# Optimization experiments

Hardware: AMD Instinct MI355X
Metric: run time of the kernel (lower is better)

Reference implementation:

```python
import jax, jax.numpy as jnp
import numpy as np

NL = 4      # num_hidden_layers
NH = 12     # self-attn heads
CH = 4      # cross-attn heads (hardcoded in module)
S = 4       # speakers per dialog
EPS = 1e-5

def layernorm(x, g, b):
    m = x.mean(-1, keepdims=True)
    v = jnp.mean((x - m) ** 2, axis=-1, keepdims=True)
    return (x - m) * jax.lax.rsqrt(v + EPS) * g + b

def self_mha(x, in_w, in_b, out_w, out_b):
    # x: [B,T,L,H] self-attention over L (the per-turn token axis)
    B, T, L, H = x.shape
    dh = H // NH
    qkv = x @ in_w + in_b                       # [B,T,L,3H]
    q, k, v = jnp.split(qkv, 3, axis=-1)
    q = q.reshape(B, T, L, NH, dh); k = k.reshape(B, T, L, NH, dh); v = v.reshape(B, T, L, NH, dh)
    s = jnp.einsum('btqhd,btkhd->bthqk', q, k) / np.sqrt(dh).astype(x.dtype)
    a = jax.nn.softmax(s, axis=-1)
    o = jnp.einsum('bthqk,btkhd->btqhd', a, v).reshape(B, T, L, H)
    return o @ out_w + out_b

def forward(input_ids, attention_mask, speaker_ids, tok_emb, pos_emb, turn_emb,
            mha_in_w, mha_in_b, mha_out_w, mha_out_b,
            ffn_w1, ffn_b1, ffn_w2, ffn_b2,
            ln1_g, ln1_b, ln2_g, ln2_b,
            gate_w, gate_b, sn_g, sn_b,
            ca_in_w, ca_in_b, ca_out_w, ca_out_b):
    B, T, L = input_ids.shape
    H = tok_emb.shape[1]
    X = tok_emb[input_ids] + pos_emb[jnp.arange(L)][None, None] + turn_emb[jnp.arange(T)][None, :, None]
    mask = attention_mask[..., None].astype(X.dtype)            # [B,T,L,1]
    onehot = (speaker_ids[..., None] == jnp.arange(S)).astype(X.dtype)  # [B,T,S]
    counts = onehot.sum(1)                                      # [B,S]
    M = jnp.zeros((B, S, H), X.dtype)                           # speaker memory
    for l in range(NL):
        m_t = jnp.einsum('bts,bsh->bth', onehot, M)             # gather memory per turn
        h = (X + m_t[:, :, None, :]) * mask                     # mask applied by zeroing inputs (as in source)
        h = self_mha(h, mha_in_w[l], mha_in_b[l], mha_out_w[l], mha_out_b[l])
        h = layernorm(h + X, ln1_g[l], ln1_b[l])
        ffn = jax.nn.gelu(h @ ffn_w1[l] + ffn_b1[l], approximate=False) @ ffn_w2[l] + ffn_b2[l]
        h = layernorm(h + ffn, ln2_g[l], ln2_b[l])
        X = h
        tc = h.mean(2)                                          # token_context [B,T,H]
        # cross-attention: each turn's context queries its dialog's speaker memory
        wq, wk, wv = jnp.split(ca_in_w[l], 3, axis=-1)
        bq, bk, bv = jnp.split(ca_in_b[l], 3)
        dh = H // CH
        q = (tc @ wq + bq).reshape(B, T, CH, dh)
        k = (M @ wk + bk).reshape(B, S, CH, dh)
        v = (M @ wv + bv).reshape(B, S, CH, dh)
        s = jnp.einsum('bthd,bshd->bhts', q, k) / np.sqrt(dh).astype(X.dtype)
        a = jax.nn.softmax(s, axis=-1)
        cc = jnp.einsum('bhts,bshd->bthd', a, v).reshape(B, T, H) @ ca_out_w[l] + ca_out_b[l]
        fused = jnp.concatenate([tc, m_t, cc], axis=-1)         # [B,T,3H]
        upd = layernorm(fused @ gate_w[l] + gate_b[l] + m_t, sn_g[l], sn_b[l])
        # scatter: per-speaker mean over that speaker's turns; untouched speakers keep old memory
        sums = jnp.einsum('bts,bth->bsh', onehot, upd)
        mean = sums / jnp.maximum(counts, 1.0)[..., None]
        M = jnp.where((counts > 0)[..., None], mean, M)
    return X, M

def setup_inputs() -> dict:
    key = jax.random.key(0)
    ks = iter(jax.random.split(key, 32))
    B, T, L, H, F, V, P = 8, 64, 64, 768, 3072, 30522, 512
    n = lambda shape: jax.random.normal(next(ks), shape, jnp.float32) * 0.02
    return {
        'input_ids': jax.random.randint(next(ks), (B, T, L), 0, V, jnp.int32),
        'attention_mask': jax.random.randint(next(ks), (B, T, L), 0, 2, jnp.int32),
        'speaker_ids': jax.random.randint(next(ks), (B, T), 0, S, jnp.int32),
        'tok_emb': n((V, H)), 'pos_emb': n((P, H)), 'turn_emb': n((P, H)),
        'mha_in_w': n((NL, H, 3 * H)), 'mha_in_b': jnp.zeros((NL, 3 * H)),
        'mha_out_w': n((NL, H, H)), 'mha_out_b': jnp.zeros((NL, H)),
        'ffn_w1': n((NL, H, F)), 'ffn_b1': jnp.zeros((NL, F)),
        'ffn_w2': n((NL, F, H)), 'ffn_b2': jnp.zeros((NL, H)),
        'ln1_g': jnp.ones((NL, H)), 'ln1_b': jnp.zeros((NL, H)),
        'ln2_g': jnp.ones((NL, H)), 'ln2_b': jnp.zeros((NL, H)),
        'gate_w': n((NL, 3 * H, H)), 'gate_b': jnp.zeros((NL, H)),
        'sn_g': jnp.ones((NL, H)), 'sn_b': jnp.zeros((NL, H)),
        'ca_in_w': n((NL, H, 3 * H)), 'ca_in_b': jnp.zeros((NL, 3 * H)),
        'ca_out_w': n((NL, H, H)), 'ca_out_b': jnp.zeros((NL, H)),
    }

def reference(input_ids, attention_mask, speaker_ids, tok_emb, pos_emb, turn_emb,
              mha_in_w, mha_in_b, mha_out_w, mha_out_b,
              ffn_w1, ffn_b1, ffn_w2, ffn_b2,
              ln1_g, ln1_b, ln2_g, ln2_b,
              gate_w, gate_b, sn_g, sn_b,
              ca_in_w, ca_in_b, ca_out_w, ca_out_b):
    return forward(input_ids, attention_mask, speaker_ids, tok_emb, pos_emb, turn_emb,
                   mha_in_w, mha_in_b, mha_out_w, mha_out_b,
                   ffn_w1, ffn_b1, ffn_w2, ffn_b2,
                   ln1_g, ln1_b, ln2_g, ln2_b,
                   gate_w, gate_b, sn_g, sn_b,
                   ca_in_w, ca_in_b, ca_out_w, ca_out_b)
```

## Files before the change

kernel.cpp:

```cpp
#include <hip/hip_runtime.h>

using u16 = unsigned short;
using u32 = unsigned int;

#define DI __device__ __forceinline__

typedef __bf16 bf16x8 __attribute__((ext_vector_type(8)));
typedef float  f32x4  __attribute__((ext_vector_type(4)));

DI float b2f(u16 u){ u32 x = ((u32)u) << 16; float f; __builtin_memcpy(&f, &x, 4); return f; }
DI u16 f2b(float f){ __bf16 h = (__bf16)f; u16 r; __builtin_memcpy(&r, &h, 2); return r; }
DI float gelu_fast(float v){
    float u = v * (0.7978845608f + 0.0356774081f * v * v);
    float e = __expf(2.0f * u);
    float t = 1.0f - 2.0f / (e + 1.0f);
    return 0.5f * v * (1.0f + t);
}

#define GLOAD16(g, l) __builtin_amdgcn_global_load_lds( \
    (const __attribute__((address_space(1))) void*)(g), \
    (__attribute__((address_space(3))) void*)(l), 16, 0, 0)

DI bf16x8 ldsr128(const u16* p) {
    bf16x8 r;
    asm volatile("ds_read_b128 %0, %1"
                 : "=v"(r)
                 : "v"((const __attribute__((address_space(3))) u16*)p));
    return r;
}

template<int EPI>
__global__ __launch_bounds__(512, 2)
void gemm256(const u16* __restrict__ A, const u16* __restrict__ Bt,
             const float* __restrict__ bias, void* __restrict__ Cout,
             int M, int N, int K)
{
    __shared__ u16 lA[3][256 * 32];
    __shared__ u16 lB[3][256 * 32];
    const int tid  = threadIdx.x;
    const int lane = tid & 63;
    const int w    = tid >> 6;
    const int wm   = w >> 2, wn = w & 3;

    const int nx = gridDim.x;
    const int nb = nx * gridDim.y;
    int bid = blockIdx.y * nx + blockIdx.x;
    if ((nb & 7) == 0) bid = ((bid & 7) * (nb >> 3)) + (bid >> 3);
    const int m0 = (bid / nx) * 256;
    const int n0 = (bid % nx) * 256;

    f32x4 acc[8][4] = {};

    const int srow = tid >> 2;
    const int scol = (((tid & 3) ^ ((tid >> 3) & 3)) * 8);
    int ar0 = m0 + srow;       if (ar0 > M - 1) ar0 = M - 1;
    int ar1 = m0 + 128 + srow; if (ar1 > M - 1) ar1 = M - 1;
    const u16* gA0 = A  + (size_t)ar0 * K + scol;
    const u16* gA1 = A  + (size_t)ar1 * K + scol;
    const u16* gB0 = Bt + (size_t)(n0 + srow) * K + scol;
    const u16* gB1 = Bt + (size_t)(n0 + 128 + srow) * K + scol;

    const int la = lane & 15, lg = lane >> 4;
    const int cp = (lg ^ ((la >> 1) & 3)) * 8;

    const int nt = K >> 5;

    #define STAGE256(buf, koff) do { \
        GLOAD16(gA0 + (koff), &lA[buf][tid * 8]); \
        GLOAD16(gA1 + (koff), &lA[buf][4096 + tid * 8]); \
        GLOAD16(gB0 + (koff), &lB[buf][tid * 8]); \
        GLOAD16(gB1 + (koff), &lB[buf][4096 + tid * 8]); \
    } while (0)

    STAGE256(0, 0);
    STAGE256(1, 32);

    int cur = 0, pre = 2;
    for (int t = 0; t < nt; ++t) {
        if (t + 1 < nt) asm volatile("s_waitcnt vmcnt(4)" ::: "memory");
        else            asm volatile("s_waitcnt vmcnt(0)" ::: "memory");
        __builtin_amdgcn_s_barrier();
        asm volatile("" ::: "memory");

        if (t + 2 < nt) STAGE256(pre, (t + 2) << 5);

        bf16x8 af[8], bfr[4];
        #pragma unroll
        for (int i = 0; i < 8; i++)
            af[i] = ldsr128(&lA[cur][(wm * 128 + i * 16 + la) * 32 + cp]);
        #pragma unroll
        for (int j = 0; j < 4; j++)
            bfr[j] = ldsr128(&lB[cur][(wn * 64 + j * 16 + la) * 32 + cp]);
        asm volatile("s_waitcnt lgkmcnt(0)" ::: "memory");
        __builtin_amdgcn_sched_barrier(0);

        __builtin_amdgcn_s_setprio(1);
        #pragma unroll
        for (int i = 0; i < 8; i++)
            #pragma unroll
            for (int j = 0; j < 4; j++)
                acc[i][j] = __builtin_amdgcn_mfma_f32_16x16x32_bf16(af[i], bfr[j], acc[i][j], 0, 0, 0);
        __builtin_amdgcn_s_setprio(0);

        cur = (cur == 2) ? 0 : cur + 1;
        pre = (pre == 2) ? 0 : pre + 1;
    }
    #undef STAGE256

    #pragma unroll
    for (int i = 0; i < 8; i++) {
        const int rowb = m0 + wm * 128 + i * 16 + lg * 4;
        #pragma unroll
        for (int j = 0; j < 4; j++) {
            const int col = n0 + wn * 64 + j * 16 + la;
            const float bv = bias[col];
            #pragma unroll
            for (int r = 0; r < 4; r++) {
                const int rr = rowb + r;
                if (rr < M) {
                    float v = acc[i][j][r] + bv;
                    if constexpr (EPI == 1) v = gelu_fast(v);
                    if constexpr (EPI == 2) ((float*)Cout)[(size_t)rr * N + col] = v;
                    else                    ((u16*)Cout)[(size_t)rr * N + col] = f2b(v);
                }
            }
        }
    }
}

template<int EPI>
__global__ __launch_bounds__(256)
void gemm_bt(const u16* __restrict__ A, const u16* __restrict__ Bt,
             const float* __restrict__ bias, void* __restrict__ Cout,
             int M, int N, int K)
{
    __shared__ u16 lA[3][128 * 32];
    __shared__ u16 lB[3][128 * 32];
    const int tid  = threadIdx.x;
    const int lane = tid & 63;
    const int w    = tid >> 6;
    const int wm   = w >> 1, wn = w & 1;

    const int nx = gridDim.x;
    const int nb = nx * gridDim.y;
    int bid = blockIdx.y * nx + blockIdx.x;
    if ((nb & 7) == 0) bid = ((bid & 7) * (nb >> 3)) + (bid >> 3);
    const int m0 = (bid / nx) * 128;
    const int n0 = (bid % nx) * 128;

    f32x4 acc[4][4] = {};

    const int srow = tid >> 2;
    const int scol = (((tid & 3) ^ ((tid >> 3) & 3)) * 8);
    int ar0 = m0 + srow;      if (ar0 > M - 1) ar0 = M - 1;
    int ar1 = m0 + 64 + srow; if (ar1 > M - 1) ar1 = M - 1;
    const u16* gA0 = A  + (size_t)ar0 * K + scol;
    const u16* gA1 = A  + (size_t)ar1 * K + scol;
    const u16* gB0 = Bt + (size_t)(n0 + srow) * K + scol;
    const u16* gB1 = Bt + (size_t)(n0 + 64 + srow) * K + scol;

    const int la = lane & 15, lg = lane >> 4;
    const int cp = (lg ^ ((la >> 1) & 3)) * 8;

    const int nt = K >> 5;

    GLOAD16(gA0,      &lA[0][tid * 8]);
    GLOAD16(gA1,      &lA[0][tid * 8 + 2048]);
    GLOAD16(gB0,      &lB[0][tid * 8]);
    GLOAD16(gB1,      &lB[0][tid * 8 + 2048]);
    GLOAD16(gA0 + 32, &lA[1][tid * 8]);
    GLOAD16(gA1 + 32, &lA[1][tid * 8 + 2048]);
    GLOAD16(gB0 + 32, &lB[1][tid * 8]);
    GLOAD16(gB1 + 32, &lB[1][tid * 8 + 2048]);

    int cur = 0, pre = 2;
    for (int t = 0; t < nt; ++t) {
        if (t + 1 < nt) asm volatile("s_waitcnt vmcnt(4)" ::: "memory");
        else            asm volatile("s_waitcnt vmcnt(0)" ::: "memory");
        __builtin_amdgcn_s_barrier();
        asm volatile("" ::: "memory");

        if (t + 2 < nt) {
            const int k0 = (t + 2) << 5;
            GLOAD16(gA0 + k0, &lA[pre][tid * 8]);
            GLOAD16(gA1 + k0, &lA[pre][tid * 8 + 2048]);
            GLOAD16(gB0 + k0, &lB[pre][tid * 8]);
            GLOAD16(gB1 + k0, &lB[pre][tid * 8 + 2048]);
        }

        bf16x8 af[4], bfr[4];
        #pragma unroll
        for (int i = 0; i < 4; i++)
            af[i] = ldsr128(&lA[cur][(wm * 64 + i * 16 + la) * 32 + cp]);
        #pragma unroll
        for (int j = 0; j < 4; j++)
            bfr[j] = ldsr128(&lB[cur][(wn * 64 + j * 16 + la) * 32 + cp]);
        asm volatile("s_waitcnt lgkmcnt(0)" ::: "memory");
        __builtin_amdgcn_sched_barrier(0);

        #pragma unroll
        for (int i = 0; i < 4; i++)
            #pragma unroll
            for (int j = 0; j < 4; j++)
                acc[i][j] = __builtin_amdgcn_mfma_f32_16x16x32_bf16(af[i], bfr[j], acc[i][j], 0, 0, 0);

        cur = (cur == 2) ? 0 : cur + 1;
        pre = (pre == 2) ? 0 : pre + 1;
    }

    #pragma unroll
    for (int i = 0; i < 4; i++) {
        const int rowb = m0 + wm * 64 + i * 16 + lg * 4;
        #pragma unroll
        for (int j = 0; j < 4; j++) {
            const int col = n0 + wn * 64 + j * 16 + la;
            const float bv = bias[col];
            #pragma unroll
            for (int r = 0; r < 4; r++) {
                const int rr = rowb + r;
                if (rr < M) {
                    float v = acc[i][j][r] + bv;
                    if constexpr (EPI == 1) v = gelu_fast(v);
                    if constexpr (EPI == 2) ((float*)Cout)[(size_t)rr * N + col] = v;
                    else                    ((u16*)Cout)[(size_t)rr * N + col] = f2b(v);
                }
            }
        }
    }
}

__global__ __launch_bounds__(256)
void transp_conv(const float* __restrict__ in, u16* __restrict__ out, int K, int N)
{
    __shared__ float tile[32][33];
    const int l = blockIdx.z;
    const float* inp = in + (size_t)l * K * N;
    u16* op = out + (size_t)l * K * N;
    const int kb = blockIdx.y * 32, nb = blockIdx.x * 32;
    const int tx = threadIdx.x, ty = threadIdx.y;
    #pragma unroll
    for (int i = 0; i < 32; i += 8)
        tile[ty + i][tx] = inp[(size_t)(kb + ty + i) * N + nb + tx];
    __syncthreads();
    #pragma unroll
    for (int i = 0; i < 32; i += 8)
        op[(size_t)(nb + ty + i) * K + kb + tx] = f2b(tile[tx][ty + i]);
}

__global__ __launch_bounds__(192)
void embed_k(const int* __restrict__ ids, const float* __restrict__ te,
             const float* __restrict__ pe, const float* __restrict__ ue,
             u16* __restrict__ X)
{
    const int tok = blockIdx.x;
    const int l = tok & 63;
    const int t = (tok >> 6) & 63;
    const int id = ids[tok];
    const int c = threadIdx.x * 4;
    float4 a = *(const float4*)&te[(size_t)id * 768 + c];
    float4 p = *(const float4*)&pe[(size_t)l * 768 + c];
    float4 u = *(const float4*)&ue[(size_t)t * 768 + c];
    ushort4 o;
    o.x = f2b(a.x + p.x + u.x); o.y = f2b(a.y + p.y + u.y);
    o.z = f2b(a.z + p.z + u.z); o.w = f2b(a.w + p.w + u.w);
    *(ushort4*)&X[(size_t)tok * 768 + c] = o;
}

__global__ __launch_bounds__(256)
void gather_mt(const float* __restrict__ M, const int* __restrict__ sid,
               float* __restrict__ mt)
{
    const int bt = blockIdx.x, b = bt >> 6, tid = threadIdx.x;
    const float* src = M + ((size_t)b * 4 + sid[bt]) * 768;
    float* dst = mt + (size_t)bt * 768;
    dst[tid] = src[tid]; dst[tid + 256] = src[tid + 256]; dst[tid + 512] = src[tid + 512];
}

__global__ __launch_bounds__(192)
void prep_ain(const u16* __restrict__ X, const float* __restrict__ mt,
              const int* __restrict__ mask, u16* __restrict__ Ain)
{
    const int tok = blockIdx.x, bt = tok >> 6;
    const float mk = (float)mask[tok];
    const int c = threadIdx.x * 4;
    ushort4 xv = *(const ushort4*)&X[(size_t)tok * 768 + c];
    float4 mv = *(const float4*)&mt[(size_t)bt * 768 + c];
    ushort4 o;
    o.x = f2b((b2f(xv.x) + mv.x) * mk); o.y = f2b((b2f(xv.y) + mv.y) * mk);
    o.z = f2b((b2f(xv.z) + mv.z) * mk); o.w = f2b((b2f(xv.w) + mv.w) * mk);
    *(ushort4*)&Ain[(size_t)tok * 768 + c] = o;
}

DI int swz(int row, int col) { return row * 64 + (((col >> 3) ^ (row & 7)) << 3) + (col & 7); }

__global__ __launch_bounds__(256)
void attn_self(const u16* __restrict__ QKV, u16* __restrict__ O)
{
    __shared__ u16 lQ[64 * 64], lK[64 * 64], lVt[64 * 64], lP[64 * 64];
    __shared__ float lS[64 * 68];
    const int bt = blockIdx.x / 12, h = blockIdx.x % 12;
    const int tid = threadIdx.x, lane = tid & 63, w = tid >> 6;
    const size_t base = (size_t)bt * 64 * 2304;

    #pragma unroll
    for (int it = 0; it < 2; ++it) {
        const int slot = it * 256 + tid;
        const int l = slot >> 3, dc = (slot & 7) * 8;
        const u16* qp = QKV + base + (size_t)l * 2304 + h * 64 + dc;
        *(uint4*)&lQ[swz(l, dc)] = *(const uint4*)qp;
        *(uint4*)&lK[swz(l, dc)] = *(const uint4*)(qp + 768);
        uint4 vv = *(const uint4*)(qp + 1536);
        u16 tmp[8]; *(uint4*)tmp = vv;
        #pragma unroll
        for (int j = 0; j < 8; j++) lVt[swz(dc + j, l)] = tmp[j];
    }
    __syncthreads();

    const int la = lane & 15, lg = lane >> 4;
    {
        f32x4 sa[4] = {};
        #pragma unroll
        for (int kh = 0; kh < 64; kh += 32) {
            bf16x8 aq = *(const bf16x8*)&lQ[swz(w * 16 + la, kh + lg * 8)];
            #pragma unroll
            for (int fn = 0; fn < 4; ++fn) {
                bf16x8 bk = *(const bf16x8*)&lK[swz(fn * 16 + la, kh + lg * 8)];
                sa[fn] = __builtin_amdgcn_mfma_f32_16x16x32_bf16(aq, bk, sa[fn], 0, 0, 0);
            }
        }
        #pragma unroll
        for (int fn = 0; fn < 4; ++fn)
            #pragma unroll
            for (int r = 0; r < 4; ++r)
                lS[(w * 16 + lg * 4 + r) * 68 + fn * 16 + la] = sa[fn][r] * 0.125f;
    }
    __syncthreads();

    {
        const int row = tid >> 2, q4 = tid & 3;
        float e[16]; float mx = -1e30f;
        #pragma unroll
        for (int j = 0; j < 16; j++) { e[j] = lS[row * 68 + q4 * 16 + j]; mx = fmaxf(mx, e[j]); }
        mx = fmaxf(mx, __shfl_xor(mx, 1)); mx = fmaxf(mx, __shfl_xor(mx, 2));
        float sm = 0.f;
        #pragma unroll
        for (int j = 0; j < 16; j++) { e[j] = __expf(e[j] - mx); sm += e[j]; }
        sm += __shfl_xor(sm, 1); sm += __shfl_xor(sm, 2);
        const float inv = 1.0f / sm;
        #pragma unroll
        for (int j = 0; j < 16; j++) lP[swz(row, q4 * 16 + j)] = f2b(e[j] * inv);
    }
    __syncthreads();

    {
        f32x4 oa[4] = {};
        #pragma unroll
        for (int kh = 0; kh < 64; kh += 32) {
            bf16x8 ap = *(const bf16x8*)&lP[swz(w * 16 + la, kh + lg * 8)];
            #pragma unroll
            for (int fn = 0; fn < 4; ++fn) {
                bf16x8 bv = *(const bf16x8*)&lVt[swz(fn * 16 + la, kh + lg * 8)];
                oa[fn] = __builtin_amdgcn_mfma_f32_16x16x32_bf16(ap, bv, oa[fn], 0, 0, 0);
            }
        }
        const size_t ob = (size_t)bt * 64 * 768 + h * 64;
        #pragma unroll
        for (int fn = 0; fn < 4; ++fn)
            #pragma unroll
            for (int r = 0; r < 4; ++r)
                O[ob + (size_t)(w * 16 + lg * 4 + r) * 768 + fn * 16 + la] = f2b(oa[fn][r]);
    }
}

DI float wave_red(float v) {
    #pragma unroll
    for (int o = 32; o > 0; o >>= 1) v += __shfl_xor(v, o);
    return v;
}

__global__ __launch_bounds__(256)
void ln_res(const u16* __restrict__ a, const u16* __restrict__ b,
            const float* __restrict__ g, const float* __restrict__ be,
            u16* __restrict__ out)
{
    __shared__ float red[8];
    const int tid = threadIdx.x;
    const size_t off = (size_t)blockIdx.x * 768;
    float x0 = b2f(a[off + tid])       + b2f(b[off + tid]);
    float x1 = b2f(a[off + tid + 256]) + b2f(b[off + tid + 256]);
    float x2 = b2f(a[off + tid + 512]) + b2f(b[off + tid + 512]);
    float s = wave_red(x0 + x1 + x2);
    float ss = wave_red(x0 * x0 + x1 * x1 + x2 * x2);
    if ((tid & 63) == 0) { red[tid >> 6] = s; red[4 + (tid >> 6)] = ss; }
    __syncthreads();
    s = red[0] + red[1] + red[2] + red[3];
    ss = red[4] + red[5] + red[6] + red[7];
    const float mean = s * (1.f / 768.f);
    const float var = fmaxf(ss * (1.f / 768.f) - mean * mean, 0.f);
    const float inv = rsqrtf(var + 1e-5f);
    out[off + tid]       = f2b((x0 - mean) * inv * g[tid]       + be[tid]);
    out[off + tid + 256] = f2b((x1 - mean) * inv * g[tid + 256] + be[tid + 256]);
    out[off + tid + 512] = f2b((x2 - mean) * inv * g[tid + 512] + be[tid + 512]);
}

__global__ __launch_bounds__(256)
void ln_upd(const float* __restrict__ a, const float* __restrict__ b,
            const float* __restrict__ g, const float* __restrict__ be,
            float* __restrict__ out)
{
    __shared__ float red[8];
    const int tid = threadIdx.x;
    const size_t off = (size_t)blockIdx.x * 768;
    float x0 = a[off + tid]       + b[off + tid];
    float x1 = a[off + tid + 256] + b[off + tid + 256];
    float x2 = a[off + tid + 512] + b[off + tid + 512];
    float s = wave_red(x0 + x1 + x2);
    float ss = wave_red(x0 * x0 + x1 * x1 + x2 * x2);
    if ((tid & 63) == 0) { red[tid >> 6] = s; red[4 + (tid >> 6)] = ss; }
    __syncthreads();
    s = red[0] + red[1] + red[2] + red[3];
    ss = red[4] + red[5] + red[6] + red[7];
    const float mean = s * (1.f / 768.f);
    const float var = fmaxf(ss * (1.f / 768.f) - mean * mean, 0.f);
    const float inv = rsqrtf(var + 1e-5f);
    out[off + tid]       = (x0 - mean) * inv * g[tid]       + be[tid];
    out[off + tid + 256] = (x1 - mean) * inv * g[tid + 256] + be[tid + 256];
    out[off + tid + 512] = (x2 - mean) * inv * g[tid + 512] + be[tid + 512];
}

__global__ __launch_bounds__(256)
void tc_mean(const u16* __restrict__ X, u16* __restrict__ tcb)
{
    const int bt = blockIdx.x, tid = threadIdx.x;
    float s0 = 0, s1 = 0, s2 = 0;
    for (int l = 0; l < 64; ++l) {
        const u16* r = X + ((size_t)bt * 64 + l) * 768;
        s0 += b2f(r[tid]); s1 += b2f(r[tid + 256]); s2 += b2f(r[tid + 512]);
    }
    tcb[(size_t)bt * 768 + tid]       = f2b(s0 * (1.f / 64.f));
    tcb[(size_t)bt * 768 + tid + 256] = f2b(s1 * (1.f / 64.f));
    tcb[(size_t)bt * 768 + tid + 512] = f2b(s2 * (1.f / 64.f));
}

__global__ __launch_bounds__(256)
void conv_bf16(const float* __restrict__ in, u16* __restrict__ out, int n)
{
    const int i = blockIdx.x * 256 + threadIdx.x;
    if (i < n) out[i] = f2b(in[i]);
}

__global__ __launch_bounds__(256)
void zero_f32(float* __restrict__ buf, int n)
{
    const int i = blockIdx.x * 256 + threadIdx.x;
    if (i < n) buf[i] = 0.f;
}

__global__ __launch_bounds__(256)
void cross_attn(const u16* __restrict__ qc, const u16* __restrict__ kvc,
                u16* __restrict__ cca)
{
    __shared__ float q[768], kk[4][768], vv[4][768], sraw[16], aw[16];
    const int bt = blockIdx.x, b = bt >> 6, tid = threadIdx.x;
    #pragma unroll
    for (int i = 0; i < 3; i++) q[tid + i * 256] = b2f(qc[(size_t)bt * 768 + tid + i * 256]);
    #pragma unroll
    for (int i = 0; i < 12; i++) {
        const int idx = i * 256 + tid;
        const int s = idx / 768, d = idx % 768;
        kk[s][d] = b2f(kvc[(size_t)(b * 4 + s) * 1536 + d]);
        vv[s][d] = b2f(kvc[(size_t)(b * 4 + s) * 1536 + 768 + d]);
    }
    __syncthreads();
    if (tid < 16) {
        const int hh = tid >> 2, s = tid & 3;
        float acc = 0.f;
        for (int d = 0; d < 192; ++d) acc += q[hh * 192 + d] * kk[s][hh * 192 + d];
        sraw[tid] = acc * 0.07216878364870323f;
    }
    __syncthreads();
    if (tid < 4) {
        float m = -1e30f;
        for (int s = 0; s < 4; s++) m = fmaxf(m, sraw[tid * 4 + s]);
        float ee[4], sm = 0.f;
        for (int s = 0; s < 4; s++) { ee[s] = __expf(sraw[tid * 4 + s] - m); sm += ee[s]; }
        for (int s = 0; s < 4; s++) aw[tid * 4 + s] = ee[s] / sm;
    }
    __syncthreads();
    #pragma unroll
    for (int i = 0; i < 3; i++) {
        const int j = tid + i * 256;
        const int hh = j / 192;
        float v = aw[hh * 4 + 0] * vv[0][j] + aw[hh * 4 + 1] * vv[1][j]
                + aw[hh * 4 + 2] * vv[2][j] + aw[hh * 4 + 3] * vv[3][j];
        cca[(size_t)bt * 768 + j] = f2b(v);
    }
}

__global__ __launch_bounds__(256)
void concat_fused(const u16* __restrict__ tcb, const float* __restrict__ mt,
                  const u16* __restrict__ ccp, u16* __restrict__ Fu)
{
    const int bt = blockIdx.x, tid = threadIdx.x;
    u16* o = Fu + (size_t)bt * 2304;
    #pragma unroll
    for (int i = 0; i < 3; i++) {
        const int j = tid + i * 256;
        o[j]        = tcb[(size_t)bt * 768 + j];
        o[768 + j]  = f2b(mt[(size_t)bt * 768 + j]);
        o[1536 + j] = ccp[(size_t)bt * 768 + j];
    }
}

__global__ __launch_bounds__(256)
void scatter_mem(const float* __restrict__ upd, const int* __restrict__ sid,
                 const float* __restrict__ counts, float* __restrict__ M)
{
    const int bs = blockIdx.x, b = bs >> 2, s = bs & 3, tid = threadIdx.x;
    const float c = counts[bs];
    #pragma unroll
    for (int i = 0; i < 3; i++) {
        const int j = tid + i * 256;
        float acc = 0.f;
        for (int t = 0; t < 64; ++t)
            if (sid[b * 64 + t] == s) acc += upd[((size_t)b * 64 + t) * 768 + j];
        if (c > 0.f) M[(size_t)bs * 768 + j] = acc / fmaxf(c, 1.f);
    }
}

__global__ void calc_counts(const int* __restrict__ sid, float* __restrict__ counts)
{
    const int tid = threadIdx.x;
    if (tid < 32) {
        const int b = tid >> 2, s = tid & 3;
        float c = 0.f;
        for (int t = 0; t < 64; ++t) c += (sid[b * 64 + t] == s) ? 1.f : 0.f;
        counts[tid] = c;
    }
}

__global__ __launch_bounds__(256)
void final_out(const u16* __restrict__ Xb, const float* __restrict__ M,
               float* __restrict__ out)
{
    const size_t i = (size_t)blockIdx.x * 256 + threadIdx.x;
    const size_t NX = 25165824ull;
    if (i < NX) out[i] = b2f(Xb[i]);
    else if (i < NX + 24576ull) out[i] = M[i - NX];
}

extern "C" void kernel_launch(void* const* d_in, const int* in_sizes, int n_in,
                              void* d_out, int out_size, void* d_ws, size_t ws_size,
                              hipStream_t stream)
{
    const int*   input_ids = (const int*)d_in[0];
    const int*   attn_mask = (const int*)d_in[1];
    const int*   sid       = (const int*)d_in[2];
    const float* tok_emb   = (const float*)d_in[3];
    const float* pos_emb   = (const float*)d_in[4];
    const float* turn_emb  = (const float*)d_in[5];
    const float* mha_in_w  = (const float*)d_in[6];
    const float* mha_in_b  = (const float*)d_in[7];
    const float* mha_out_w = (const float*)d_in[8];
    const float* mha_out_b = (const float*)d_in[9];
    const float* ffn_w1    = (const float*)d_in[10];
    const float* ffn_b1    = (const float*)d_in[11];
    const float* ffn_w2    = (const float*)d_in[12];
    const float* ffn_b2    = (const float*)d_in[13];
    const float* ln1_g     = (const float*)d_in[14];
    const float* ln1_b     = (const float*)d_in[15];
    const float* ln2_g     = (const float*)d_in[16];
    const float* ln2_b     = (const float*)d_in[17];
    const float* gate_w    = (const float*)d_in[18];
    const float* gate_b    = (const float*)d_in[19];
    const float* sn_g      = (const float*)d_in[20];
    const float* sn_b      = (const float*)d_in[21];
    const float* ca_in_w   = (const float*)d_in[22];
    const float* ca_in_b   = (const float*)d_in[23];
    const float* ca_out_w  = (const float*)d_in[24];
    const float* ca_out_b  = (const float*)d_in[25];
    (void)in_sizes; (void)n_in; (void)out_size;

    const size_t MB = 1ull << 20;
    int NCA, NCF; bool allW;
    if      (ws_size >= 460 * MB) { NCA = 2; NCF = 1; allW = true;  }
    else if (ws_size >= 255 * MB) { NCA = 2; NCF = 2; allW = false; }
    else                          { NCA = 4; NCF = 4; allW = false; }
    const int MRA = 32768 / NCA;
    const int MRF = 32768 / NCF;
    const size_t wl = allW ? 4 : 1;

    char* p = (char*)d_ws;
    auto alloc = [&](size_t n) { void* r = p; p += (n + 255) & ~(size_t)255; return r; };
    u16*   Xb    = (u16*)alloc(50331648);
    u16*   Hb    = (u16*)alloc(50331648);
    u16*   WqkvT = (u16*)alloc(wl * 3538944);
    u16*   WoT   = (u16*)alloc(wl * 1179648);
    u16*   W1T   = (u16*)alloc(wl * 4718592);
    u16*   W2T   = (u16*)alloc(wl * 4718592);
    u16*   WgT   = (u16*)alloc(wl * 3538944);
    u16*   WcaT  = (u16*)alloc(wl * 3538944);
    u16*   WcoT  = (u16*)alloc(wl * 1179648);
    float* mt    = (float*)alloc(1572864);
    u16*   tcb   = (u16*)alloc(786432);
    u16*   Mb    = (u16*)alloc(49152);
    u16*   qc    = (u16*)alloc(786432);
    u16*   kvc   = (u16*)alloc(98304);
    u16*   cca   = (u16*)alloc(786432);
    u16*   ccp   = (u16*)alloc(786432);
    u16*   Fu    = (u16*)alloc(2359296);
    float* gout  = (float*)alloc(1572864);
    float* upd   = (float*)alloc(1572864);
    float* cnts  = (float*)alloc(256);
    float* M     = (float*)alloc(98304);

    u16 *A, *QKVb, *Gb;
    if (NCF == 1) {
        A    = (u16*)alloc(50331648);
        Gb   = (u16*)alloc(201326592);
        QKVb = (u16*)d_out;
    } else if (NCF == 2) {
        A    = (u16*)alloc(50331648);
        QKVb = (u16*)alloc((size_t)MRA * 2304 * 2);
        Gb   = (u16*)d_out;
    } else {
        Gb   = (u16*)alloc((size_t)MRF * 3072 * 2);
        A    = (u16*)d_out;
        QKVb = (u16*)d_out + 25165824;
    }
    u16* Obuf = Gb;

    zero_f32<<<96, 256, 0, stream>>>(M, 24576);
    calc_counts<<<1, 64, 0, stream>>>(sid, cnts);
    embed_k<<<32768, 192, 0, stream>>>(input_ids, tok_emb, pos_emb, turn_emb, Xb);

    if (allW) {
        transp_conv<<<dim3(72, 24, 4), dim3(32, 8), 0, stream>>>(mha_in_w,  WqkvT, 768, 2304);
        transp_conv<<<dim3(24, 24, 4), dim3(32, 8), 0, stream>>>(mha_out_w, WoT,   768, 768);
        transp_conv<<<dim3(96, 24, 4), dim3(32, 8), 0, stream>>>(ffn_w1,    W1T,   768, 3072);
        transp_conv<<<dim3(24, 96, 4), dim3(32, 8), 0, stream>>>(ffn_w2,    W2T,  3072, 768);
        transp_conv<<<dim3(24, 72, 4), dim3(32, 8), 0, stream>>>(gate_w,    WgT,  2304, 768);
        transp_conv<<<dim3(72, 24, 4), dim3(32, 8), 0, stream>>>(ca_in_w,   WcaT,  768, 2304);
        transp_conv<<<dim3(24, 24, 4), dim3(32, 8), 0, stream>>>(ca_out_w,  WcoT,  768, 768);
    }

    for (int l = 0; l < 4; ++l) {
        if (!allW) {
            transp_conv<<<dim3(72, 24), dim3(32, 8), 0, stream>>>(mha_in_w  + (size_t)l * 768 * 2304, WqkvT, 768, 2304);
            transp_conv<<<dim3(24, 24), dim3(32, 8), 0, stream>>>(mha_out_w + (size_t)l * 768 * 768,  WoT,   768, 768);
            transp_conv<<<dim3(96, 24), dim3(32, 8), 0, stream>>>(ffn_w1    + (size_t)l * 768 * 3072, W1T,   768, 3072);
            transp_conv<<<dim3(24, 96), dim3(32, 8), 0, stream>>>(ffn_w2    + (size_t)l * 3072 * 768, W2T,  3072, 768);
            transp_conv<<<dim3(24, 72), dim3(32, 8), 0, stream>>>(gate_w    + (size_t)l * 2304 * 768, WgT,  2304, 768);
            transp_conv<<<dim3(72, 24), dim3(32, 8), 0, stream>>>(ca_in_w   + (size_t)l * 768 * 2304, WcaT,  768, 2304);
            transp_conv<<<dim3(24, 24), dim3(32, 8), 0, stream>>>(ca_out_w  + (size_t)l * 768 * 768,  WcoT,  768, 768);
        }
        const u16* Wqkv_l = WqkvT + (size_t)(allW ? l : 0) * 2304 * 768;
        const u16* Wo_l   = WoT   + (size_t)(allW ? l : 0) * 768 * 768;
        const u16* W1_l   = W1T   + (size_t)(allW ? l : 0) * 768 * 3072;
        const u16* W2_l   = W2T   + (size_t)(allW ? l : 0) * 3072 * 768;
        const u16* Wg_l   = WgT   + (size_t)(allW ? l : 0) * 2304 * 768;
        const u16* Wca_l  = WcaT  + (size_t)(allW ? l : 0) * 768 * 2304;
        const u16* Wco_l  = WcoT  + (size_t)(allW ? l : 0) * 768 * 768;

        gather_mt<<<512, 256, 0, stream>>>(M, sid, mt);
        prep_ain<<<32768, 192, 0, stream>>>(Xb, mt, attn_mask, A);

        for (int c = 0; c < NCA; ++c) {
            u16* Ac = A + (size_t)c * MRA * 768;
            gemm256<0><<<dim3(9, MRA / 256), 512, 0, stream>>>(Ac, Wqkv_l, mha_in_b + l * 2304, QKVb, MRA, 2304, 768);
            attn_self<<<(MRA / 64) * 12, 256, 0, stream>>>(QKVb, Obuf);
            gemm256<0><<<dim3(3, MRA / 256), 512, 0, stream>>>(Obuf, Wo_l, mha_out_b + l * 768, Ac, MRA, 768, 768);
        }
        ln_res<<<32768, 256, 0, stream>>>(A, Xb, ln1_g + l * 768, ln1_b + l * 768, Hb);

        for (int c = 0; c < NCF; ++c) {
            u16* Hc = Hb + (size_t)c * MRF * 768;
            u16* Ac = A  + (size_t)c * MRF * 768;
            gemm256<1><<<dim3(12, MRF / 256), 512, 0, stream>>>(Hc, W1_l, ffn_b1 + l * 3072, Gb, MRF, 3072, 768);
            gemm256<0><<<dim3(3, MRF / 256), 512, 0, stream>>>(Gb, W2_l, ffn_b2 + l * 768, Ac, MRF, 768, 3072);
        }
        ln_res<<<32768, 256, 0, stream>>>(A, Hb, ln2_g + l * 768, ln2_b + l * 768, Xb);

        tc_mean<<<512, 256, 0, stream>>>(Xb, tcb);
        conv_bf16<<<96, 256, 0, stream>>>(M, Mb, 24576);
        gemm_bt<0><<<dim3(6, 4), 256, 0, stream>>>(tcb, Wca_l, ca_in_b + l * 2304, qc, 512, 768, 768);
        gemm_bt<0><<<dim3(12, 1), 256, 0, stream>>>(Mb, Wca_l + 768 * 768, ca_in_b + l * 2304 + 768, kvc, 32, 1536, 768);
        cross_attn<<<512, 256, 0, stream>>>(qc, kvc, cca);
        gemm_bt<0><<<dim3(6, 4), 256, 0, stream>>>(cca, Wco_l, ca_out_b + l * 768, ccp, 512, 768, 768);
        concat_fused<<<512, 256, 0, stream>>>(tcb, mt, ccp, Fu);
        gemm_bt<2><<<dim3(6, 4), 256, 0, stream>>>(Fu, Wg_l, gate_b + l * 768, gout, 512, 768, 2304);
        ln_upd<<<512, 256, 0, stream>>>(gout, mt, sn_g + l * 768, sn_b + l * 768, upd);
        scatter_mem<<<32, 256, 0, stream>>>(upd, sid, cnts, M);
    }

    final_out<<<98400, 256, 0, stream>>>(Xb, M, (float*)d_out);
}
```

Measured before the change: 4.256 ms.

## Switch gemm256 to BK=64 double-buffered LDS pipeline with 8-way swizzle

The GEMM mainloop moves from a triple-buffered 32-wide K tile to a double-buffered 64-wide K tile. Each iteration now issues two MFMA sub-steps per barrier, and the LDS layout uses a 3-bit XOR swizzle on 64-element rows. The aim is to halve the number of barriers and loop iterations and to raise global load granularity. LDS use rises to 128KB per block, which forces launch_bounds occupancy down to 1 block per CU. A full vmcnt(0) wait each iteration removes the two-deep prefetch slack the old version had.

Result: no change. 4.208 ms (-1.1%).

```diff
diff --git a/kernel.cpp b/kernel.cpp
--- a/kernel.cpp
+++ b/kernel.cpp
@@ -30,13 +30,13 @@
 }
 
 template<int EPI>
-__global__ __launch_bounds__(512, 2)
+__global__ __launch_bounds__(512, 1)
 void gemm256(const u16* __restrict__ A, const u16* __restrict__ Bt,
              const float* __restrict__ bias, void* __restrict__ Cout,
              int M, int N, int K)
 {
-    __shared__ u16 lA[3][256 * 32];
-    __shared__ u16 lB[3][256 * 32];
+    __shared__ u16 lA[2][256 * 64];
+    __shared__ u16 lB[2][256 * 64];
     const int tid  = threadIdx.x;
     const int lane = tid & 63;
     const int w    = tid >> 6;
@@ -51,61 +51,64 @@
 
     f32x4 acc[8][4] = {};
 
-    const int srow = tid >> 2;
-    const int scol = (((tid & 3) ^ ((tid >> 3) & 3)) * 8);
-    int ar0 = m0 + srow;       if (ar0 > M - 1) ar0 = M - 1;
-    int ar1 = m0 + 128 + srow; if (ar1 > M - 1) ar1 = M - 1;
-    const u16* gA0 = A  + (size_t)ar0 * K + scol;
-    const u16* gA1 = A  + (size_t)ar1 * K + scol;
-    const u16* gB0 = Bt + (size_t)(n0 + srow) * K + scol;
-    const u16* gB1 = Bt + (size_t)(n0 + 128 + srow) * K + scol;
+    const int srowb = w * 32 + (lane >> 3);
+    const int csrc  = ((lane & 7) ^ ((lane >> 3) & 7)) * 8;
+    const u16* gA[4];
+    const u16* gB[4];
+    #pragma unroll
+    for (int i = 0; i < 4; ++i) {
+        int ra = m0 + srowb + i * 8; if (ra > M - 1) ra = M - 1;
+        gA[i] = A  + (size_t)ra * K + csrc;
+        gB[i] = Bt + (size_t)(n0 + srowb + i * 8) * K + csrc;
+    }
 
     const int la = lane & 15, lg = lane >> 4;
-    const int cp = (lg ^ ((la >> 1) & 3)) * 8;
-
-    const int nt = K >> 5;
-
-    #define STAGE256(buf, koff) do { \
-        GLOAD16(gA0 + (koff), &lA[buf][tid * 8]); \
-        GLOAD16(gA1 + (koff), &lA[buf][4096 + tid * 8]); \
-        GLOAD16(gB0 + (koff), &lB[buf][tid * 8]); \
-        GLOAD16(gB1 + (koff), &lB[buf][4096 + tid * 8]); \
+    const int nt = K >> 6;
+
+    #define STAGE(buf, k0) do { \
+        _Pragma("unroll") \
+        for (int i = 0; i < 4; ++i) { \
+            GLOAD16(gA[i] + (k0), &lA[buf][(w * 256 + i * 64 + lane) * 8]); \
+            GLOAD16(gB[i] + (k0), &lB[buf][(w * 256 + i * 64 + lane) * 8]); \
+        } \
     } while (0)
 
-    STAGE256(0, 0);
-    STAGE256(1, 32);
-
-    int cur = 0, pre = 2;
+    STAGE(0, 0);
+
+    int cur = 0;
     for (int t = 0; t < nt; ++t) {
-        if (t + 1 < nt) asm volatile("s_waitcnt vmcnt(4)" ::: "memory");
-        else            asm volatile("s_waitcnt vmcnt(0)" ::: "memory");
+        asm volatile("s_waitcnt vmcnt(0)" ::: "memory");
         __builtin_amdgcn_s_barrier();
         asm volatile("" ::: "memory");
 
-        if (t + 2 < nt) STAGE256(pre, (t + 2) << 5);
-
-        bf16x8 af[8], bfr[4];
-        #pragma unroll
-        for (int i = 0; i < 8; i++)
-            af[i] = ldsr128(&lA[cur][(wm * 128 + i * 16 + la) * 32 + cp]);
-        #pragma unroll
-        for (int j = 0; j < 4; j++)
-            bfr[j] = ldsr128(&lB[cur][(wn * 64 + j * 16 + la) * 32 + cp]);
-        asm volatile("s_waitcnt lgkmcnt(0)" ::: "memory");
-        __builtin_amdgcn_sched_barrier(0);
-
-        __builtin_amdgcn_s_setprio(1);
-        #pragma unroll
-        for (int i = 0; i < 8; i++)
+        if (t + 1 < nt) STAGE(cur ^ 1, (t + 1) << 6);
+
+        #pragma unroll
+        for (int ks = 0; ks < 2; ++ks) {
+            bf16x8 af[8], bfr[4];
+            #pragma unroll
+            for (int i = 0; i < 8; i++)
+                af[i] = ldsr128(&lA[cur][(wm * 128 + i * 16 + la) * 64
+                                         + (((ks * 4 + lg) ^ (la & 7)) * 8)]);
             #pragma unroll
             for (int j = 0; j < 4; j++)
-                acc[i][j] = __builtin_amdgcn_mfma_f32_16x16x32_bf16(af[i], bfr[j], acc[i][j], 0, 0, 0);
-        __builtin_amdgcn_s_setprio(0);
-
-        cur = (cur == 2) ? 0 : cur + 1;
-        pre = (pre == 2) ? 0 : pre + 1;
-    }
-    #undef STAGE256
+                bfr[j] = ldsr128(&lB[cur][(wn * 64 + j * 16 + la) * 64
+                                          + (((ks * 4 + lg) ^ (la & 7)) * 8)]);
+            asm volatile("s_waitcnt lgkmcnt(0)" ::: "memory");
+            __builtin_amdgcn_sched_barrier(0);
+
+            __builtin_amdgcn_s_setprio(1);
+            #pragma unroll
+            for (int i = 0; i < 8; i++)
+                #pragma unroll
+                for (int j = 0; j < 4; j++)
+                    acc[i][j] = __builtin_amdgcn_mfma_f32_16x16x32_bf16(af[i], bfr[j], acc[i][j], 0, 0, 0);
+            __builtin_amdgcn_s_setprio(0);
+        }
+
+        cur ^= 1;
+    }
+    #undef STAGE
 
     #pragma unroll
     for (int i = 0; i < 8; i++) {
```
